# Performance work log

Measured on AMD Instinct MI355X. Metric: run time of the kernel, lower is better.

## Reference

```python
import jax, jax.numpy as jnp
import numpy as np

N_NODES = 50000
N_EDGES = 800000
N_GRAPHS = 512
IN_F = 128
HEADS = 8
HEAD_C = 8
OUT_F = HEADS * HEAD_C  # 64
NEG_SLOPE = 0.2


def setup_inputs() -> dict:
    key = jax.random.key(0)
    ks = jax.random.split(key, 10)
    x = jax.random.normal(ks[0], (N_NODES, IN_F), dtype=jnp.float32)
    edge_index = jax.random.randint(ks[1], (2, N_EDGES), 0, N_NODES, dtype=jnp.int64)
    batch = jnp.sort(jax.random.randint(ks[2], (N_NODES,), 0, N_GRAPHS, dtype=jnp.int64))
    s = 0.05
    W = jax.random.normal(ks[3], (IN_F, OUT_F), dtype=jnp.float32) * s
    att_src = jax.random.normal(ks[4], (HEADS, HEAD_C), dtype=jnp.float32) * s
    att_dst = jax.random.normal(ks[5], (HEADS, HEAD_C), dtype=jnp.float32) * s
    bias = jax.random.normal(ks[6], (OUT_F,), dtype=jnp.float32) * s
    pool_w_rel = jax.random.normal(ks[7], (OUT_F, 1), dtype=jnp.float32) * s
    pool_b_rel = jax.random.normal(ks[8], (1,), dtype=jnp.float32) * s
    pool_w_root = jax.random.normal(ks[9], (OUT_F, 1), dtype=jnp.float32) * s
    return {"x": x, "edge_index": edge_index, "batch": batch, "W": W,
            "att_src": att_src, "att_dst": att_dst, "bias": bias,
            "pool_w_rel": pool_w_rel, "pool_b_rel": pool_b_rel,
            "pool_w_root": pool_w_root}


def _segment_softmax(e, seg, num_segments):
    # numerically stable scatter-softmax over segments
    m = jax.ops.segment_max(e, seg, num_segments=num_segments)
    ex = jnp.exp(e - m[seg])
    denom = jax.ops.segment_sum(ex, seg, num_segments=num_segments)
    return ex / (denom[seg] + 1e-16)


def reference(x, edge_index, batch, W, att_src, att_dst, bias,
              pool_w_rel, pool_b_rel, pool_w_root):
    N = N_NODES
    # ---- GATConv (concat heads, self-loops added, LeakyReLU 0.2) ----
    loops = jnp.arange(N, dtype=edge_index.dtype)
    src = jnp.concatenate([edge_index[0], loops])
    dst = jnp.concatenate([edge_index[1], loops])
    h = (x @ W).reshape(N, HEADS, HEAD_C)                 # [N,H,C]
    a_s = jnp.einsum('nhc,hc->nh', h, att_src)            # [N,H]
    a_d = jnp.einsum('nhc,hc->nh', h, att_dst)
    e = jax.nn.leaky_relu(a_s[src] + a_d[dst], NEG_SLOPE) # [E+N,H]
    alpha = _segment_softmax(e, dst, N)                   # softmax over incoming edges
    out = jax.ops.segment_sum(h[src] * alpha[:, :, None], dst, num_segments=N)
    out = out.reshape(N, OUT_F) + bias                    # [N,64]
    # ---- SAGPooling(min_score=-1): GraphConv score + per-graph softmax,
    #      all nodes kept (softmax scores > -1), features scaled by score ----
    s2, d2 = edge_index[0], edge_index[1]
    aggr = jax.ops.segment_sum(out[s2], d2, num_segments=N)  # add-aggregation
    score = (aggr @ pool_w_rel + pool_b_rel + out @ pool_w_root)[:, 0]  # [N]
    score = _segment_softmax(score, batch, N_GRAPHS)
    att_x = out * score[:, None]
    # ---- global_add_pool ----
    g = jax.ops.segment_sum(att_x, batch, num_segments=N_GRAPHS)  # [G,64]
    return out, g
```

## Files before the change

### kernel.cpp

```cpp
#include <hip/hip_runtime.h>

#define NN 50000
#define NE 800000
#define NG 512
#define INF_ 128
#define OUTF 64
#define CAP 64

#define NPART 4
#define PSIZE 12500
#define NCHUNK 250
#define CHUNKE 3200

#define GEMM_BLOCKS ((NN + 63) / 64)
#define FRONT_BLOCKS (NCHUNK * 8)

#define XSTRIDE 136

__device__ __forceinline__ unsigned short f2bf(float f) {
    unsigned int u = __float_as_uint(f);
    unsigned int r = (u + 0x7fffu + ((u >> 16) & 1u)) >> 16;
    return (unsigned short)r;
}
__device__ __forceinline__ float bf2f(unsigned int lo16) {
    return __uint_as_float(lo16 << 16);
}

__global__ __launch_bounds__(256) void k_front(
    const int* __restrict__ ei, int* __restrict__ deg,
    unsigned short* __restrict__ adj, float* __restrict__ gden,
    float* __restrict__ g_num,
    const float* __restrict__ x, const float* __restrict__ W,
    const float* __restrict__ att_src, const float* __restrict__ att_dst,
    unsigned short* __restrict__ hb, float* __restrict__ a_s,
    float* __restrict__ a_d)
{
    __shared__ unsigned short Ws[INF_ * OUTF];
    __shared__ unsigned short Xs[64 * XSTRIDE];

    {
        int idx = blockIdx.x * 256 + threadIdx.x;
        if (idx < NG) gden[idx] = 0.f;
        else if (idx < NG + NG * OUTF) g_num[idx - NG] = 0.f;
    }

    const int r   = blockIdx.x & 7;
    const int oct = blockIdx.x >> 3;

    if (r < NPART) {
        const int lo = r * PSIZE;
        const int e0 = oct * CHUNKE;
        const int e1 = (e0 + CHUNKE < NE) ? e0 + CHUNKE : NE;
        for (int e = e0 + threadIdx.x; e < e1; e += 256) {
            int d = ei[NE + e];
            unsigned int rel = (unsigned int)(d - lo);
            if (rel < PSIZE) {
                int s = ei[e];
                int p = atomicAdd(&deg[d], 1);
                if (p < CAP) adj[(size_t)d * CAP + p] = (unsigned short)s;
            }
        }
        return;
    }

    const int bid = oct * 4 + (r - 4);
    if (bid >= GEMM_BLOCKS) return;
    const int n0 = bid * 64;

    #pragma unroll
    for (int it = 0; it < 8; it++) {
        int i = it * 256 + threadIdx.x;
        float4 v = ((const float4*)W)[i];
        ushort4 b;
        b.x = f2bf(v.x); b.y = f2bf(v.y); b.z = f2bf(v.z); b.w = f2bf(v.w);
        ((ushort4*)Ws)[i] = b;
    }

    #pragma unroll
    for (int it = 0; it < 8; it++) {
        int idx = it * 256 + threadIdx.x;
        int row = idx >> 5;
        int c4  = idx & 31;
        int n = n0 + row;
        if (n > NN - 1) n = NN - 1;
        float4 v = ((const float4*)(x + (size_t)n * INF_))[c4];
        ushort4 b;
        b.x = f2bf(v.x); b.y = f2bf(v.y); b.z = f2bf(v.z); b.w = f2bf(v.w);
        *(ushort4*)&Xs[row * XSTRIDE + c4 * 4] = b;
    }
    __syncthreads();

    const int colg = threadIdx.x & 15;
    const int rowg = threadIdx.x >> 4;

    const unsigned short* xr[4];
    #pragma unroll
    for (int rr = 0; rr < 4; rr++)
        xr[rr] = &Xs[(rowg * 4 + rr) * XSTRIDE];

    float acc[4][4];
    #pragma unroll
    for (int rr = 0; rr < 4; rr++)
        #pragma unroll
        for (int c = 0; c < 4; c++) acc[rr][c] = 0.f;

    for (int k8 = 0; k8 < INF_ / 8; k8++) {
        uint4 xv[4];
        #pragma unroll
        for (int rr = 0; rr < 4; rr++)
            xv[rr] = *(const uint4*)(xr[rr] + k8 * 8);
        #pragma unroll
        for (int kk = 0; kk < 8; kk++) {
            uint2 wu = *(const uint2*)&Ws[(k8 * 8 + kk) * OUTF + colg * 4];
            float w0 = bf2f(wu.x & 0xffffu), w1 = bf2f(wu.x >> 16);
            float w2 = bf2f(wu.y & 0xffffu), w3 = bf2f(wu.y >> 16);
            #pragma unroll
            for (int rr = 0; rr < 4; rr++) {
                unsigned int pair = ((const unsigned int*)&xv[rr])[kk >> 1];
                float xs_ = bf2f((kk & 1) ? (pair >> 16) : (pair & 0xffffu));
                acc[rr][0] = fmaf(xs_, w0, acc[rr][0]);
                acc[rr][1] = fmaf(xs_, w1, acc[rr][1]);
                acc[rr][2] = fmaf(xs_, w2, acc[rr][2]);
                acc[rr][3] = fmaf(xs_, w3, acc[rr][3]);
            }
        }
    }

    float asv[4], adv[4];
    #pragma unroll
    for (int c = 0; c < 4; c++) {
        asv[c] = att_src[colg * 4 + c];
        adv[c] = att_dst[colg * 4 + c];
    }

    #pragma unroll
    for (int rr = 0; rr < 4; rr++) {
        const int n = n0 + rowg * 4 + rr;
        const bool valid = (n < NN);
        if (valid) {
            ushort4 o;
            o.x = f2bf(acc[rr][0]); o.y = f2bf(acc[rr][1]);
            o.z = f2bf(acc[rr][2]); o.w = f2bf(acc[rr][3]);
            ((ushort4*)(hb + (size_t)n * OUTF))[colg] = o;
        }
        float vs = acc[rr][0]*asv[0] + acc[rr][1]*asv[1] + acc[rr][2]*asv[2] + acc[rr][3]*asv[3];
        float vd = acc[rr][0]*adv[0] + acc[rr][1]*adv[1] + acc[rr][2]*adv[2] + acc[rr][3]*adv[3];
        vs += __shfl_xor(vs, 1, 64);
        vd += __shfl_xor(vd, 1, 64);
        if (valid && !(colg & 1)) {
            a_s[n * 8 + (colg >> 1)] = vs;
            a_d[n * 8 + (colg >> 1)] = vd;
        }
    }
}

__global__ __launch_bounds__(256) void k_aggr(
    const unsigned short* __restrict__ hb, const float* __restrict__ a_s,
    const float* __restrict__ a_d, const int* __restrict__ deg,
    const unsigned short* __restrict__ adj, const float* __restrict__ bias,
    const float* __restrict__ w_rel, const float* __restrict__ w_root,
    float* __restrict__ out, float* __restrict__ t_rel, float* __restrict__ t_root)
{
    const int wid  = threadIdx.x >> 6;
    const int lane = threadIdx.x & 63;
    const int g    = lane >> 3;
    const int c8   = lane & 7;
    const int n    = blockIdx.x * 4 + wid;
    if (n >= NN) return;

    const float ad_n = a_d[n * 8 + c8];

    float acc[8];
    #pragma unroll
    for (int k = 0; k < 8; k++) acc[k] = 0.f;
    float den = 0.f;

    if (g == 0) {
        float e0 = a_s[n * 8 + c8] + ad_n;
        e0 = e0 > 0.f ? e0 : 0.2f * e0;
        float ex0 = __expf(e0);
        uint4 hv = *(const uint4*)(hb + (size_t)n * OUTF + c8 * 8);
        acc[0] = ex0 * bf2f(hv.x & 0xffffu); acc[1] = ex0 * bf2f(hv.x >> 16);
        acc[2] = ex0 * bf2f(hv.y & 0xffffu); acc[3] = ex0 * bf2f(hv.y >> 16);
        acc[4] = ex0 * bf2f(hv.z & 0xffffu); acc[5] = ex0 * bf2f(hv.z >> 16);
        acc[6] = ex0 * bf2f(hv.w & 0xffffu); acc[7] = ex0 * bf2f(hv.w >> 16);
        den = ex0;
    }

    const int cnt = min(deg[n], CAP);
    const unsigned short* lst = adj + (size_t)n * CAP;
    for (int i = g; i < cnt; i += 8) {
        int s = lst[i];
        float as = a_s[s * 8 + c8];
        uint4 hv = *(const uint4*)(hb + (size_t)s * OUTF + c8 * 8);
        float e = as + ad_n;
        e = e > 0.f ? e : 0.2f * e;
        float ex = __expf(e);
        acc[0] = fmaf(ex, bf2f(hv.x & 0xffffu), acc[0]);
        acc[1] = fmaf(ex, bf2f(hv.x >> 16),     acc[1]);
        acc[2] = fmaf(ex, bf2f(hv.y & 0xffffu), acc[2]);
        acc[3] = fmaf(ex, bf2f(hv.y >> 16),     acc[3]);
        acc[4] = fmaf(ex, bf2f(hv.z & 0xffffu), acc[4]);
        acc[5] = fmaf(ex, bf2f(hv.z >> 16),     acc[5]);
        acc[6] = fmaf(ex, bf2f(hv.w & 0xffffu), acc[6]);
        acc[7] = fmaf(ex, bf2f(hv.w >> 16),     acc[7]);
        den += ex;
    }

    #pragma unroll
    for (int m = 8; m < 64; m <<= 1) {
        den += __shfl_xor(den, m, 64);
        #pragma unroll
        for (int k = 0; k < 8; k++) acc[k] += __shfl_xor(acc[k], m, 64);
    }

    const float inv = 1.f / (den + 1e-16f);
    float o[8];
    #pragma unroll
    for (int k = 0; k < 8; k++) o[k] = acc[k] * inv + bias[c8 * 8 + k];

    if (g == 0) {
        float4 o0 = make_float4(o[0], o[1], o[2], o[3]);
        float4 o1 = make_float4(o[4], o[5], o[6], o[7]);
        float4* op = (float4*)(out + (size_t)n * OUTF + c8 * 8);
        op[0] = o0; op[1] = o1;
    }

    float vr = 0.f, vt = 0.f;
    #pragma unroll
    for (int k = 0; k < 8; k++) {
        vr = fmaf(o[k], w_rel[c8 * 8 + k], vr);
        vt = fmaf(o[k], w_root[c8 * 8 + k], vt);
    }
    #pragma unroll
    for (int m = 1; m < 8; m <<= 1) {
        vr += __shfl_xor(vr, m, 64);
        vt += __shfl_xor(vt, m, 64);
    }
    if (lane == 0) { t_rel[n] = vr; t_root[n] = vt; }
}

__global__ __launch_bounds__(256) void k_score_pool(
    const int* __restrict__ deg, const unsigned short* __restrict__ adj,
    const float* __restrict__ t_rel, const float* __restrict__ t_root,
    const float* __restrict__ pool_b, const int* __restrict__ batch,
    const float* __restrict__ out,
    float* __restrict__ gden, float* __restrict__ g_num)
{
    __shared__ float ex_s[32];
    __shared__ int   b_s[32];

    const int wid  = threadIdx.x >> 6;
    const int lane = threadIdx.x & 63;
    const int sub  = lane >> 3;
    const int g    = lane & 7;
    const int base_n = blockIdx.x * 32;
    const int n    = base_n + wid * 8 + sub;

    const int cnt = (n < NN) ? min(deg[n], CAP) : 0;
    const unsigned short* lst = adj + (size_t)n * CAP;
    float acc = 0.f;
    for (int i = g; i < cnt; i += 8) acc += t_rel[lst[i]];
    #pragma unroll
    for (int m = 1; m < 8; m <<= 1) acc += __shfl_xor(acc, m, 64);

    if (g == 0) {
        const int slot = wid * 8 + sub;
        if (n < NN) {
            float ex = __expf(acc + t_root[n] + pool_b[0]);
            ex_s[slot] = ex;
            b_s[slot]  = batch[n];
        } else {
            ex_s[slot] = 0.f;
            b_s[slot]  = -1;
        }
    }
    __syncthreads();

    if (threadIdx.x == 0) {
        float racc = 0.f;
        int bcur = -1;
        for (int i = 0; i < 32; i++) {
            int b = b_s[i];
            if (b != bcur) {
                if (bcur >= 0) atomicAdd(&gden[bcur], racc);
                bcur = b; racc = 0.f;
            }
            racc += ex_s[i];
        }
        if (bcur >= 0) atomicAdd(&gden[bcur], racc);
    }

    const int j = lane;
    float facc = 0.f;
    int bcur = -1;
    for (int i = 0; i < 8; i++) {
        const int slot = wid * 8 + i;
        const int n2 = base_n + slot;
        if (n2 >= NN) break;
        int b = b_s[slot];
        if (b != bcur) {
            if (bcur >= 0) atomicAdd(&g_num[bcur * OUTF + j], facc);
            bcur = b; facc = 0.f;
        }
        facc = fmaf(out[(size_t)n2 * OUTF + j], ex_s[slot], facc);
    }
    if (bcur >= 0) atomicAdd(&g_num[bcur * OUTF + j], facc);
}

__global__ __launch_bounds__(256) void k_gfinal(
    const float* __restrict__ g_num, const float* __restrict__ gden,
    float* __restrict__ g)
{
    int i = blockIdx.x * 256 + threadIdx.x;
    if (i < NG * OUTF) g[i] = g_num[i] / (gden[i >> 6] + 1e-16f);
}

extern "C" void kernel_launch(void* const* d_in, const int* in_sizes, int n_in,
                              void* d_out, int out_size, void* d_ws, size_t ws_size,
                              hipStream_t stream)
{
    const float* x        = (const float*)d_in[0];
    const int*   ei       = (const int*)  d_in[1];
    const int*   batch    = (const int*)  d_in[2];
    const float* W        = (const float*)d_in[3];
    const float* att_src  = (const float*)d_in[4];
    const float* att_dst  = (const float*)d_in[5];
    const float* bias     = (const float*)d_in[6];
    const float* w_rel    = (const float*)d_in[7];
    const float* pool_b   = (const float*)d_in[8];
    const float* w_root   = (const float*)d_in[9];

    float* out_nodes = (float*)d_out;
    float* g_out     = (float*)d_out + (size_t)NN * OUTF;

    char* base = (char*)d_ws;
    unsigned short* hb = (unsigned short*)(base);
    float* a_s       = (float*)(base +  6400000);
    float* a_d       = (float*)(base +  8000000);
    float* t_rel     = (float*)(base +  9600000);
    float* t_root    = (float*)(base +  9800000);
    float* gden      = (float*)(base + 10000000);
    float* g_num     = (float*)(base + 10002048);
    int*   deg       = (int*)  (base + 10133120);
    unsigned short* adjl = (unsigned short*)(base + 10333120);

    hipMemsetAsync(deg, 0, (size_t)NN * 4, stream);

    k_front<<<FRONT_BLOCKS, 256, 0, stream>>>(
        ei, deg, adjl, gden, g_num,
        x, W, att_src, att_dst, hb, a_s, a_d);
    k_aggr<<<(NN + 3) / 4, 256, 0, stream>>>(hb, a_s, a_d, deg, adjl, bias,
                                             w_rel, w_root, out_nodes, t_rel, t_root);
    k_score_pool<<<(NN + 31) / 32, 256, 0, stream>>>(deg, adjl, t_rel, t_root,
                                                     pool_b, batch, out_nodes,
                                                     gden, g_num);
    k_gfinal<<<(NG * OUTF + 255) / 256, 256, 0, stream>>>(g_num, gden, g_out);
}
```

Baseline: 174.0 us.

## Build adjacency via two-pass bucketed sort with shared-memory local scatter

Replaces direct global atomic scatter of edges into per-node adjacency lists with a two-phase build. First, edge chunks are locally counting-sorted into 512-node buckets and written to per-bucket global buffers. Then a new kernel builds each half-bucket's adjacency in shared memory and writes it out coalesced. This aims to cut scattered global atomics and random 2-byte writes, at the cost of an extra kernel launch, an intermediate buffer and fixed bucket capacity limits.

```diff
diff --git a/kernel.cpp b/kernel.cpp
--- a/kernel.cpp
+++ b/kernel.cpp
@@ -7,13 +7,15 @@
 #define OUTF 64
 #define CAP 64
 
-#define NPART 4
-#define PSIZE 12500
+#define NPB 98
+#define BSHIFT 9
+#define BNODES 512
+#define BCAP 9216
 #define NCHUNK 250
-#define CHUNKE 3200
+#define BCH 3200
 
 #define GEMM_BLOCKS ((NN + 63) / 64)
-#define FRONT_BLOCKS (NCHUNK * 8)
+#define FRONT_BLOCKS 1032
 
 #define XSTRIDE 136
 
@@ -27,16 +29,27 @@
 }
 
 __global__ __launch_bounds__(256) void k_front(
-    const int* __restrict__ ei, int* __restrict__ deg,
-    unsigned short* __restrict__ adj, float* __restrict__ gden,
+    const int* __restrict__ ei, int* __restrict__ bcnt,
+    unsigned int* __restrict__ ebuf, float* __restrict__ gden,
     float* __restrict__ g_num,
     const float* __restrict__ x, const float* __restrict__ W,
     const float* __restrict__ att_src, const float* __restrict__ att_dst,
     unsigned short* __restrict__ hb, float* __restrict__ a_s,
     float* __restrict__ a_d)
 {
-    __shared__ unsigned short Ws[INF_ * OUTF];
-    __shared__ unsigned short Xs[64 * XSTRIDE];
+    __shared__ union {
+        struct {
+            unsigned short Ws[INF_ * OUTF];
+            unsigned short Xs[64 * XSTRIDE];
+        } g;
+        struct {
+            int hist[128];
+            int bofs[128];
+            int goff[128];
+            unsigned int pk[BCH];
+            unsigned int ord[BCH];
+        } b;
+    } sm;
 
     {
         int idx = blockIdx.x * 256 + threadIdx.x;
@@ -44,28 +57,75 @@
         else if (idx < NG + NG * OUTF) g_num[idx - NG] = 0.f;
     }
 
-    const int r   = blockIdx.x & 7;
-    const int oct = blockIdx.x >> 3;
-
-    if (r < NPART) {
-        const int lo = r * PSIZE;
-        const int e0 = oct * CHUNKE;
-        const int e1 = (e0 + CHUNKE < NE) ? e0 + CHUNKE : NE;
-        for (int e = e0 + threadIdx.x; e < e1; e += 256) {
-            int d = ei[NE + e];
-            unsigned int rel = (unsigned int)(d - lo);
-            if (rel < PSIZE) {
+    const int t = threadIdx.x;
+    int gemmIdx;
+    if (blockIdx.x < 1000) {
+        const int oct = blockIdx.x >> 2;
+        const int r   = blockIdx.x & 3;
+        if (r == 0) {
+            if (t < 128) sm.b.hist[t] = 0;
+            __syncthreads();
+
+            const int e0 = oct * BCH;
+            for (int i = t; i < BCH; i += 256) {
+                int e = e0 + i;
                 int s = ei[e];
-                int p = atomicAdd(&deg[d], 1);
-                if (p < CAP) adj[(size_t)d * CAP + p] = (unsigned short)s;
-            }
-        }
-        return;
-    }
-
-    const int bid = oct * 4 + (r - 4);
-    if (bid >= GEMM_BLOCKS) return;
-    const int n0 = bid * 64;
+                int d = ei[NE + e];
+                int bb = d >> BSHIFT;
+                unsigned int v = ((unsigned int)bb << 25) |
+                                 ((unsigned int)(d & (BNODES - 1)) << 16) |
+                                 (unsigned int)s;
+                sm.b.pk[i] = v;
+                atomicAdd(&sm.b.hist[bb], 1);
+            }
+            __syncthreads();
+
+            int cntv = 0;
+            if (t < 128) {
+                cntv = sm.b.hist[t];
+                sm.b.bofs[t] = cntv;
+                sm.b.goff[t] = (t < NPB) ? atomicAdd(&bcnt[t], cntv) : 0;
+            }
+            __syncthreads();
+            for (int off = 1; off < 128; off <<= 1) {
+                int v2;
+                if (t < 128) {
+                    v2 = sm.b.bofs[t];
+                    if (t >= off) v2 += sm.b.bofs[t - off];
+                }
+                __syncthreads();
+                if (t < 128) sm.b.bofs[t] = v2;
+                __syncthreads();
+            }
+            if (t < 128) {
+                int excl = sm.b.bofs[t] - cntv;
+                sm.b.bofs[t] = excl;
+                sm.b.hist[t] = excl;
+            }
+            __syncthreads();
+
+            for (int i = t; i < BCH; i += 256) {
+                unsigned int v = sm.b.pk[i];
+                int bb = v >> 25;
+                int p = atomicAdd(&sm.b.hist[bb], 1);
+                sm.b.ord[p] = v;
+            }
+            __syncthreads();
+
+            for (int i = t; i < BCH; i += 256) {
+                unsigned int v = sm.b.ord[i];
+                int bb = v >> 25;
+                int gp = sm.b.goff[bb] + (i - sm.b.bofs[bb]);
+                if (gp < BCAP) ebuf[(size_t)bb * BCAP + gp] = v;
+            }
+            return;
+        }
+        gemmIdx = oct * 3 + (r - 1);
+    } else {
+        gemmIdx = 750 + (blockIdx.x - 1000);
+    }
+
+    const int n0 = gemmIdx * 64;
 
     #pragma unroll
     for (int it = 0; it < 8; it++) {
@@ -73,7 +133,7 @@
         float4 v = ((const float4*)W)[i];
         ushort4 b;
         b.x = f2bf(v.x); b.y = f2bf(v.y); b.z = f2bf(v.z); b.w = f2bf(v.w);
-        ((ushort4*)Ws)[i] = b;
+        ((ushort4*)sm.g.Ws)[i] = b;
     }
 
     #pragma unroll
@@ -86,7 +146,7 @@
         float4 v = ((const float4*)(x + (size_t)n * INF_))[c4];
         ushort4 b;
         b.x = f2bf(v.x); b.y = f2bf(v.y); b.z = f2bf(v.z); b.w = f2bf(v.w);
-        *(ushort4*)&Xs[row * XSTRIDE + c4 * 4] = b;
+        *(ushort4*)&sm.g.Xs[row * XSTRIDE + c4 * 4] = b;
     }
     __syncthreads();
 
@@ -96,7 +156,7 @@
     const unsigned short* xr[4];
     #pragma unroll
     for (int rr = 0; rr < 4; rr++)
-        xr[rr] = &Xs[(rowg * 4 + rr) * XSTRIDE];
+        xr[rr] = &sm.g.Xs[(rowg * 4 + rr) * XSTRIDE];
 
     float acc[4][4];
     #pragma unroll
@@ -111,7 +171,7 @@
             xv[rr] = *(const uint4*)(xr[rr] + k8 * 8);
         #pragma unroll
         for (int kk = 0; kk < 8; kk++) {
-            uint2 wu = *(const uint2*)&Ws[(k8 * 8 + kk) * OUTF + colg * 4];
+            uint2 wu = *(const uint2*)&sm.g.Ws[(k8 * 8 + kk) * OUTF + colg * 4];
             float w0 = bf2f(wu.x & 0xffffu), w1 = bf2f(wu.x >> 16);
             float w2 = bf2f(wu.y & 0xffffu), w3 = bf2f(wu.y >> 16);
             #pragma unroll
@@ -151,6 +211,47 @@
             a_s[n * 8 + (colg >> 1)] = vs;
             a_d[n * 8 + (colg >> 1)] = vd;
         }
+    }
+}
+
+#define BHALF 256
+__global__ __launch_bounds__(256) void k_build(
+    const unsigned int* __restrict__ ebuf, const int* __restrict__ bcnt,
+    int* __restrict__ deg, unsigned short* __restrict__ adj)
+{
+    __shared__ unsigned short ladj[BHALF * CAP];
+    __shared__ int ldeg[BHALF];
+
+    const int b    = blockIdx.x >> 1;
+    const int half = blockIdx.x & 1;
+    const int rlo  = half * BHALF;
+    const int t    = threadIdx.x;
+
+    if (t < BHALF) ldeg[t] = 0;
+    __syncthreads();
+
+    const int cnt = min(bcnt[b], BCAP);
+    const unsigned int* eb = ebuf + (size_t)b * BCAP;
+    for (int i = t; i < cnt; i += 256) {
+        unsigned int v = eb[i];
+        int drel = (v >> 16) & (BNODES - 1);
+        unsigned int rr = (unsigned int)(drel - rlo);
+        if (rr < BHALF) {
+            int p = atomicAdd(&ldeg[rr], 1);
+            if (p < CAP) ladj[rr * CAP + p] = (unsigned short)(v & 0xffffu);
+        }
+    }
+    __syncthreads();
+
+    const int n0 = b * BNODES + rlo;
+    if (t < BHALF) {
+        int n = n0 + t;
+        if (n < NN) deg[n] = ldeg[t];
+    }
+    for (int i = t; i < BHALF * CAP / 8; i += 256) {
+        int n = n0 + (i >> 3);
+        if (n < NN)
+            ((uint4*)(adj + (size_t)n * CAP))[i & 7] = ((const uint4*)ladj)[i];
     }
 }
 
@@ -344,12 +445,15 @@
     float* g_num     = (float*)(base + 10002048);
     int*   deg       = (int*)  (base + 10133120);
     unsigned short* adjl = (unsigned short*)(base + 10333120);
-
-    hipMemsetAsync(deg, 0, (size_t)NN * 4, stream);
+    unsigned int* ebuf = (unsigned int*)(base + 16733120);
+    int*   bcnt      = (int*)  (base + 20345792);
+
+    hipMemsetAsync(bcnt, 0, 512, stream);
 
     k_front<<<FRONT_BLOCKS, 256, 0, stream>>>(
-        ei, deg, adjl, gden, g_num,
+        ei, bcnt, ebuf, gden, g_num,
         x, W, att_src, att_dst, hb, a_s, a_d);
+    k_build<<<NPB * 2, 256, 0, stream>>>(ebuf, bcnt, deg, adjl);
     k_aggr<<<(NN + 3) / 4, 256, 0, stream>>>(hb, a_s, a_d, deg, adjl, bias,
                                              w_rel, w_root, out_nodes, t_rel, t_root);
     k_score_pool<<<(NN + 31) / 32, 256, 0, stream>>>(deg, adjl, t_rel, t_root,
```

Result: no change. 173.6 us (-0.2%).
